# Kernel tuning notes

Hardware: AMD Instinct MI355X
Metric: run time of the kernel (lower is better)

## Reference

```python
import jax, jax.numpy as jnp
import numpy as np

B, T, C = 4, 2048, 1024
H, D = 16, 64  # num_heads, head_dim; H*D == C

def setup_inputs() -> dict:
    key = jax.random.key(0)
    ks = jax.random.split(key, 5)
    s = 0.02
    return {
        "x": jax.random.normal(ks[0], (B, T, C), dtype=jnp.float32),
        "W_qkv": jax.random.normal(ks[1], (C, 3 * C), dtype=jnp.float32) * s,
        "b_qkv": jnp.zeros((3 * C,), dtype=jnp.float32),
        "W_out": jax.random.normal(ks[2], (C, C), dtype=jnp.float32) * s,
        "b_out": jnp.zeros((C,), dtype=jnp.float32),
    }

def reference(x, W_qkv, b_qkv, W_out, b_out):
    Bx, Tx, Cx = x.shape
    qkv = x @ W_qkv + b_qkv                       # [B,T,3C]
    q, k, v = jnp.split(qkv, 3, axis=-1)
    def heads(t):
        return t.reshape(Bx, Tx, H, D).transpose(0, 2, 1, 3)  # [B,H,T,D]
    q, k, v = heads(q), heads(k), heads(v)
    scale = 1.0 / jnp.sqrt(jnp.float32(D))
    attn = jnp.einsum('bhqd,bhkd->bhqk', q, k) * scale
    causal = jnp.tril(jnp.ones((Tx, Tx), dtype=bool))  # True = keep
    attn = jnp.where(causal, attn, -jnp.inf)
    attn = jax.nn.softmax(attn, axis=-1)
    out = jnp.einsum('bhqk,bhkd->bhqd', attn, v)  # [B,H,T,D]
    out = out.transpose(0, 2, 1, 3).reshape(Bx, Tx, Cx)
    return out @ W_out + b_out
```

## Files before the change

### kernel.cpp

```cpp
#include <hip/hip_runtime.h>
#include <math.h>

typedef unsigned short u16;
using bf16x8   = __attribute__((ext_vector_type(8))) __bf16;
using floatx4  = __attribute__((ext_vector_type(4))) float;
using ushortx8 = __attribute__((ext_vector_type(8))) unsigned short;
using ushortx4 = __attribute__((ext_vector_type(4))) unsigned short;
using uintx4   = __attribute__((ext_vector_type(4))) unsigned int;

static __device__ __forceinline__ u16 f2bf(float f) {
  return (u16)((__float_as_uint(f) + 0x8000u) >> 16);
}
static __device__ __forceinline__ unsigned int pk2bf(float lo, float hi) {
  return __builtin_amdgcn_perm(__float_as_uint(hi) + 0x8000u,
                               __float_as_uint(lo) + 0x8000u, 0x07060302u);
}
static __device__ __forceinline__ void gload_lds16(const void* g, void* l) {
  __builtin_amdgcn_global_load_lds(
      (const __attribute__((address_space(1))) unsigned int*)g,
      (__attribute__((address_space(3))) unsigned int*)l, 16, 0, 0);
}

__global__ __launch_bounds__(256) void cvt_bf16(const float* __restrict__ x,
                                                u16* __restrict__ y) {
  const int i = (blockIdx.x * 256 + threadIdx.x) * 8;
  floatx4 f0 = *(const floatx4*)(x + i);
  floatx4 f1 = *(const floatx4*)(x + i + 4);
  uintx4 u;
  u[0] = pk2bf(f0[0], f0[1]); u[1] = pk2bf(f0[2], f0[3]);
  u[2] = pk2bf(f1[0], f1[1]); u[3] = pk2bf(f1[2], f1[3]);
  *(uintx4*)(y + i) = u;
}

__global__ __launch_bounds__(256) void transW(const float* __restrict__ W,
                                              u16* __restrict__ WT, int K, int N) {
  __shared__ float tile[64][68];
  const int t = threadIdx.x;
  const int kb = blockIdx.y * 64, nb = blockIdx.x * 64;
  {
    const int kl = t >> 2, nc = (t & 3) * 16;
    const float* src = W + (size_t)(kb + kl) * N + nb + nc;
    #pragma unroll
    for (int c = 0; c < 4; c++)
      *(floatx4*)&tile[kl][nc + c * 4] = *(const floatx4*)(src + c * 4);
  }
  __syncthreads();
  {
    const int nl = t >> 2, kc = (t & 3) * 16;
    uintx4 u0, u1;
    #pragma unroll
    for (int j = 0; j < 4; j++)
      u0[j] = pk2bf(tile[kc + 2 * j][nl], tile[kc + 2 * j + 1][nl]);
    #pragma unroll
    for (int j = 0; j < 4; j++)
      u1[j] = pk2bf(tile[kc + 8 + 2 * j][nl], tile[kc + 9 + 2 * j][nl]);
    u16* dst = WT + (size_t)(nb + nl) * K + kb + kc;
    *(uintx4*)dst = u0;
    *(uintx4*)(dst + 8) = u1;
  }
}

template <int OUT>
__global__ __launch_bounds__(256) void gemm128(
    const u16* __restrict__ A, const u16* __restrict__ Bt,
    const float* __restrict__ bias,
    u16* __restrict__ Qb, u16* __restrict__ Kb, u16* __restrict__ Vt,
    float* __restrict__ Out, int N, int K)
{
  __shared__ u16 As[128 * 64];
  __shared__ u16 Bs[128 * 64];

  const int tid  = threadIdx.x;
  const int wave = tid >> 6, lane = tid & 63;
  const int quad = lane >> 4, l15 = lane & 15;
  const int lrow = lane >> 3;
  const int scol = ((lane & 7) ^ lrow) * 8;

  const int rowBase = blockIdx.y * 128;
  const int colBase = blockIdx.x * 128;
  const int wRow = (wave >> 1) * 64;
  const int wCol = (wave & 1) * 64;

  floatx4 acc[4][4];
  #pragma unroll
  for (int mt = 0; mt < 4; mt++)
    #pragma unroll
    for (int nt = 0; nt < 4; nt++)
      acc[mt][nt] = floatx4{0.f, 0.f, 0.f, 0.f};

  const u16* Ap = A  + (size_t)(rowBase + (wave * 4) * 8 + lrow) * K + scol;
  const u16* Bp = Bt + (size_t)(colBase + (wave * 4) * 8 + lrow) * K + scol;

  for (int k0 = 0; k0 < K; k0 += 64) {
    __syncthreads();
    #pragma unroll
    for (int i = 0; i < 4; i++) {
      const int c = wave * 4 + i;
      gload_lds16(Ap + (size_t)(i * 8) * K + k0, &As[c * 512]);
      gload_lds16(Bp + (size_t)(i * 8) * K + k0, &Bs[c * 512]);
    }
    __syncthreads();

    #pragma unroll
    for (int ks = 0; ks < 2; ks++) {
      bf16x8 a[4], b[4];
      #pragma unroll
      for (int mt = 0; mt < 4; mt++) {
        const int row = wRow + mt * 16 + l15;
        a[mt] = *(const bf16x8*)&As[row * 64 + ((((ks << 2) | quad) ^ (l15 & 7)) << 3)];
      }
      #pragma unroll
      for (int nt = 0; nt < 4; nt++) {
        const int row = wCol + nt * 16 + l15;
        b[nt] = *(const bf16x8*)&Bs[row * 64 + ((((ks << 2) | quad) ^ (l15 & 7)) << 3)];
      }
      #pragma unroll
      for (int mt = 0; mt < 4; mt++)
        #pragma unroll
        for (int nt = 0; nt < 4; nt++)
          acc[mt][nt] = __builtin_amdgcn_mfma_f32_16x16x32_bf16(a[mt], b[nt], acc[mt][nt], 0, 0, 0);
    }
  }

  if constexpr (OUT == 0) {
    const int which = colBase >> 10;
    const int cb = colBase & 1023;
    const float qscale = 0.18033688011112042f;
    #pragma unroll
    for (int mt = 0; mt < 4; mt++) {
      const int gm0 = rowBase + wRow + mt * 16 + quad * 4;
      const int bb = gm0 >> 11, t0 = gm0 & 2047;
      #pragma unroll
      for (int nt = 0; nt < 4; nt++) {
        const int gn = colBase + wCol + nt * 16 + l15;
        const int gl = cb + wCol + nt * 16 + l15;
        const float bv = bias[gn];
        const int h = gl >> 6, d = gl & 63;
        const int bh = bb * 16 + h;
        if (which == 2) {
          ushortx4 pk;
          #pragma unroll
          for (int r = 0; r < 4; r++) pk[r] = f2bf(acc[mt][nt][r] + bv);
          *(ushortx4*)&Vt[((size_t)bh * 64 + d) * 2048 + t0] = pk;
        } else if (which == 0) {
          #pragma unroll
          for (int r = 0; r < 4; r++)
            Qb[((size_t)bh * 2048 + t0 + r) * 64 + d] = f2bf((acc[mt][nt][r] + bv) * qscale);
        } else {
          #pragma unroll
          for (int r = 0; r < 4; r++)
            Kb[((size_t)bh * 2048 + t0 + r) * 64 + d] = f2bf(acc[mt][nt][r] + bv);
        }
      }
    }
  } else {
    #pragma unroll
    for (int mt = 0; mt < 4; mt++)
      #pragma unroll
      for (int nt = 0; nt < 4; nt++) {
        const int gm = rowBase + wRow + mt * 16 + quad * 4;
        const int gn = colBase + wCol + nt * 16 + l15;
        const float bv = bias[gn];
        #pragma unroll
        for (int r = 0; r < 4; r++)
          Out[(size_t)(gm + r) * N + gn] = acc[mt][nt][r] + bv;
      }
  }
}

__global__ __launch_bounds__(256) void attn_fa(
    const u16* __restrict__ Qb, const u16* __restrict__ Kb,
    const u16* __restrict__ Vt, u16* __restrict__ Ob)
{
  __shared__ u16 Qs[128 * 64], Ks[64 * 64], Vs[64 * 64];
  __shared__ u16 Ps[4][32][72];

  const int tid  = threadIdx.x;
  const int wave = tid >> 6, lane = tid & 63;
  const int quad = lane >> 4, l15 = lane & 15;
  const int lrow = lane >> 3;
  const int scol = ((lane & 7) ^ lrow) * 8;

  const int bh    = blockIdx.x;
  const int qt    = 15 - (int)blockIdx.y;
  const int qbase = qt * 128;

  const u16* Qp = Qb + (size_t)bh * 2048 * 64;
  const u16* Kp = Kb + (size_t)bh * 2048 * 64;
  const u16* Vp = Vt + (size_t)bh * 64 * 2048;

  #pragma unroll
  for (int i = 0; i < 4; i++) {
    const int c = wave * 4 + i;
    gload_lds16(Qp + (size_t)(qbase + c * 8 + lrow) * 64 + scol, &Qs[c * 512]);
  }
  __syncthreads();

  const int swA0 = (quad ^ (l15 & 7)) * 8;
  const int swA1 = ((4 + quad) ^ (l15 & 7)) * 8;
  bf16x8 aq[2][2];
  #pragma unroll
  for (int mt = 0; mt < 2; mt++) {
    const int row = wave * 32 + mt * 16 + l15;
    aq[mt][0] = *(const bf16x8*)&Qs[row * 64 + swA0];
    aq[mt][1] = *(const bf16x8*)&Qs[row * 64 + swA1];
  }

  floatx4 o[2][4];
  #pragma unroll
  for (int mt = 0; mt < 2; mt++)
    #pragma unroll
    for (int dt = 0; dt < 4; dt++) o[mt][dt] = floatx4{0.f, 0.f, 0.f, 0.f};
  float lstat[2][4] = {{0.f, 0.f, 0.f, 0.f}, {0.f, 0.f, 0.f, 0.f}};

  const int rowmax = qbase + wave * 32 + 31;
  const int nk = 2 * qt + 2;
  for (int kt = 0; kt < nk; kt++) {
    const int kbase = kt * 64;
    __syncthreads();
    #pragma unroll
    for (int i = 0; i < 2; i++) {
      const int c = wave * 2 + i;
      gload_lds16(Kp + (size_t)(kbase + c * 8 + lrow) * 64 + scol, &Ks[c * 512]);
      gload_lds16(Vp + (size_t)(c * 8 + lrow) * 2048 + kbase + scol, &Vs[c * 512]);
    }
    __syncthreads();

    if (kbase > rowmax) continue;

    #pragma unroll
    for (int mt = 0; mt < 2; mt++) {
      const int rowmin = qbase + wave * 32 + mt * 16;
      const bool needmask = (kbase + 63 > rowmin);

      floatx4 s[4];
      #pragma unroll
      for (int ct = 0; ct < 4; ct++) {
        const int row = ct * 16 + l15;
        const bf16x8 b0 = *(const bf16x8*)&Ks[row * 64 + swA0];
        const bf16x8 b1 = *(const bf16x8*)&Ks[row * 64 + swA1];
        floatx4 z = floatx4{0.f, 0.f, 0.f, 0.f};
        z     = __builtin_amdgcn_mfma_f32_16x16x32_bf16(aq[mt][0], b0, z, 0, 0, 0);
        s[ct] = __builtin_amdgcn_mfma_f32_16x16x32_bf16(aq[mt][1], b1, z, 0, 0, 0);
      }

      #pragma unroll
      for (int r = 0; r < 4; r++) {
        const int qi = rowmin + quad * 4 + r;
        float ps = 0.f;
        #pragma unroll
        for (int ct = 0; ct < 4; ct++) {
          float p = exp2f(s[ct][r]);
          if (needmask && (kbase + ct * 16 + l15 > qi)) p = 0.f;
          ps += p;
          Ps[wave][mt * 16 + quad * 4 + r][ct * 16 + l15] = f2bf(p);
        }
        lstat[mt][r] += ps;
      }

      const bf16x8 pa0 = *(const bf16x8*)&Ps[wave][mt * 16 + l15][quad * 8];
      const bf16x8 pa1 = *(const bf16x8*)&Ps[wave][mt * 16 + l15][32 + quad * 8];
      #pragma unroll
      for (int dt = 0; dt < 4; dt++) {
        const int row = dt * 16 + l15;
        const bf16x8 v0 = *(const bf16x8*)&Vs[row * 64 + swA0];
        const bf16x8 v1 = *(const bf16x8*)&Vs[row * 64 + swA1];
        o[mt][dt] = __builtin_amdgcn_mfma_f32_16x16x32_bf16(pa0, v0, o[mt][dt], 0, 0, 0);
        o[mt][dt] = __builtin_amdgcn_mfma_f32_16x16x32_bf16(pa1, v1, o[mt][dt], 0, 0, 0);
      }
    }
  }

  const int bb = bh >> 4, h = bh & 15;
  #pragma unroll
  for (int mt = 0; mt < 2; mt++)
    #pragma unroll
    for (int r = 0; r < 4; r++) {
      float l = lstat[mt][r];
      #pragma unroll
      for (int off = 1; off < 16; off <<= 1) l += __shfl_xor(l, off, 16);
      const float linv = 1.0f / l;
      const int t = qbase + wave * 32 + mt * 16 + quad * 4 + r;
      #pragma unroll
      for (int dt = 0; dt < 4; dt++)
        Ob[((size_t)(bb * 2048 + t)) * 1024 + h * 64 + dt * 16 + l15] =
            f2bf(o[mt][dt][r] * linv);
    }
}

extern "C" void kernel_launch(void* const* d_in, const int* in_sizes, int n_in,
                              void* d_out, int out_size, void* d_ws, size_t ws_size,
                              hipStream_t stream) {
  const float* x    = (const float*)d_in[0];
  const float* Wqkv = (const float*)d_in[1];
  const float* bqkv = (const float*)d_in[2];
  const float* Wout = (const float*)d_in[3];
  const float* bout = (const float*)d_in[4];

  const size_t NB = (size_t)8192 * 1024;
  u16* Xb  = (u16*)d_ws;
  u16* WqT = Xb + NB;
  u16* Qb  = WqT + (size_t)3072 * 1024;
  u16* Kb  = Qb + NB;
  u16* Vt  = Kb + NB;

  cvt_bf16<<<4096, 256, 0, stream>>>(x, Xb);
  transW<<<dim3(48, 16), 256, 0, stream>>>(Wqkv, WqT, 1024, 3072);
  gemm128<0><<<dim3(24, 64), 256, 0, stream>>>(
      Xb, WqT, bqkv, Qb, Kb, Vt, nullptr, 3072, 1024);
  attn_fa<<<dim3(64, 16), 256, 0, stream>>>(Qb, Kb, Vt, Xb);
  transW<<<dim3(16, 16), 256, 0, stream>>>(Wout, WqT, 1024, 1024);
  gemm128<1><<<dim3(8, 64), 256, 0, stream>>>(
      Xb, WqT, bout, nullptr, nullptr, nullptr, (float*)d_out, 1024, 1024);
}
```

Baseline: 269.1 us.

## Compute transposed attention scores so P stores and output writes are vectorized

Swaps the MFMA operand order so each lane holds four consecutive key columns of S^T for one query row. P can then be written to LDS as packed 8-byte stores, row sums reduce with two shuffles instead of four, and the output is written as packed bf16 pairs. The separate P buffer is dropped and P now reuses the Q tile's LDS region after Q is moved into registers, which cuts LDS use and may help occupancy. A per-16-row causal skip is also added to avoid fully masked sub-tiles.

Measured after the change: 251.2 us. -6.6%, faster.

```diff
diff --git a/kernel.cpp b/kernel.cpp
--- a/kernel.cpp
+++ b/kernel.cpp
@@ -7,6 +7,7 @@
 using ushortx8 = __attribute__((ext_vector_type(8))) unsigned short;
 using ushortx4 = __attribute__((ext_vector_type(4))) unsigned short;
 using uintx4   = __attribute__((ext_vector_type(4))) unsigned int;
+using uintx2   = __attribute__((ext_vector_type(2))) unsigned int;
 
 static __device__ __forceinline__ u16 f2bf(float f) {
   return (u16)((__float_as_uint(f) + 0x8000u) >> 16);
@@ -172,8 +173,8 @@
     const u16* __restrict__ Qb, const u16* __restrict__ Kb,
     const u16* __restrict__ Vt, u16* __restrict__ Ob)
 {
-  __shared__ u16 Qs[128 * 64], Ks[64 * 64], Vs[64 * 64];
-  __shared__ u16 Ps[4][32][72];
+  __shared__ u16 Qs[128 * 64];
+  __shared__ u16 Ks[64 * 64], Vs[64 * 64];
 
   const int tid  = threadIdx.x;
   const int wave = tid >> 6, lane = tid & 63;
@@ -181,6 +182,8 @@
   const int lrow = lane >> 3;
   const int scol = ((lane & 7) ^ lrow) * 8;
 
+  u16* Pt = &Qs[wave * 16 * 72];
+
   const int bh    = blockIdx.x;
   const int qt    = 15 - (int)blockIdx.y;
   const int qbase = qt * 128;
@@ -211,7 +214,7 @@
   for (int mt = 0; mt < 2; mt++)
     #pragma unroll
     for (int dt = 0; dt < 4; dt++) o[mt][dt] = floatx4{0.f, 0.f, 0.f, 0.f};
-  float lstat[2][4] = {{0.f, 0.f, 0.f, 0.f}, {0.f, 0.f, 0.f, 0.f}};
+  float lsum[2] = {0.f, 0.f};
 
   const int rowmax = qbase + wave * 32 + 31;
   const int nk = 2 * qt + 2;
@@ -231,61 +234,71 @@
     #pragma unroll
     for (int mt = 0; mt < 2; mt++) {
       const int rowmin = qbase + wave * 32 + mt * 16;
+      if (kbase > rowmin + 15) continue;
       const bool needmask = (kbase + 63 > rowmin);
 
-      floatx4 s[4];
+      floatx4 st[4];
       #pragma unroll
       for (int ct = 0; ct < 4; ct++) {
         const int row = ct * 16 + l15;
-        const bf16x8 b0 = *(const bf16x8*)&Ks[row * 64 + swA0];
-        const bf16x8 b1 = *(const bf16x8*)&Ks[row * 64 + swA1];
+        const bf16x8 k0 = *(const bf16x8*)&Ks[row * 64 + swA0];
+        const bf16x8 k1 = *(const bf16x8*)&Ks[row * 64 + swA1];
         floatx4 z = floatx4{0.f, 0.f, 0.f, 0.f};
-        z     = __builtin_amdgcn_mfma_f32_16x16x32_bf16(aq[mt][0], b0, z, 0, 0, 0);
-        s[ct] = __builtin_amdgcn_mfma_f32_16x16x32_bf16(aq[mt][1], b1, z, 0, 0, 0);
-      }
-
-      #pragma unroll
-      for (int r = 0; r < 4; r++) {
-        const int qi = rowmin + quad * 4 + r;
-        float ps = 0.f;
-        #pragma unroll
-        for (int ct = 0; ct < 4; ct++) {
-          float p = exp2f(s[ct][r]);
-          if (needmask && (kbase + ct * 16 + l15 > qi)) p = 0.f;
-          ps += p;
-          Ps[wave][mt * 16 + quad * 4 + r][ct * 16 + l15] = f2bf(p);
+        z      = __builtin_amdgcn_mfma_f32_16x16x32_bf16(k0, aq[mt][0], z, 0, 0, 0);
+        st[ct] = __builtin_amdgcn_mfma_f32_16x16x32_bf16(k1, aq[mt][1], z, 0, 0, 0);
+      }
+
+      const int qg = rowmin + l15;
+      float ls = 0.f;
+      #pragma unroll
+      for (int ct = 0; ct < 4; ct++) {
+        float p0 = exp2f(st[ct][0]), p1 = exp2f(st[ct][1]);
+        float p2 = exp2f(st[ct][2]), p3 = exp2f(st[ct][3]);
+        if (needmask) {
+          const int k0i = kbase + ct * 16 + quad * 4;
+          if (k0i + 0 > qg) p0 = 0.f;
+          if (k0i + 1 > qg) p1 = 0.f;
+          if (k0i + 2 > qg) p2 = 0.f;
+          if (k0i + 3 > qg) p3 = 0.f;
         }
-        lstat[mt][r] += ps;
-      }
-
-      const bf16x8 pa0 = *(const bf16x8*)&Ps[wave][mt * 16 + l15][quad * 8];
-      const bf16x8 pa1 = *(const bf16x8*)&Ps[wave][mt * 16 + l15][32 + quad * 8];
+        ls += (p0 + p1) + (p2 + p3);
+        uintx2 w;
+        w[0] = pk2bf(p0, p1);
+        w[1] = pk2bf(p2, p3);
+        *(uintx2*)&Pt[l15 * 72 + ct * 16 + quad * 4] = w;
+      }
+      lsum[mt] += ls;
+
+      const bf16x8 pb0 = *(const bf16x8*)&Pt[l15 * 72 + quad * 8];
+      const bf16x8 pb1 = *(const bf16x8*)&Pt[l15 * 72 + 32 + quad * 8];
       #pragma unroll
       for (int dt = 0; dt < 4; dt++) {
         const int row = dt * 16 + l15;
         const bf16x8 v0 = *(const bf16x8*)&Vs[row * 64 + swA0];
         const bf16x8 v1 = *(const bf16x8*)&Vs[row * 64 + swA1];
-        o[mt][dt] = __builtin_amdgcn_mfma_f32_16x16x32_bf16(pa0, v0, o[mt][dt], 0, 0, 0);
-        o[mt][dt] = __builtin_amdgcn_mfma_f32_16x16x32_bf16(pa1, v1, o[mt][dt], 0, 0, 0);
+        o[mt][dt] = __builtin_amdgcn_mfma_f32_16x16x32_bf16(v0, pb0, o[mt][dt], 0, 0, 0);
+        o[mt][dt] = __builtin_amdgcn_mfma_f32_16x16x32_bf16(v1, pb1, o[mt][dt], 0, 0, 0);
       }
     }
   }
 
   const int bb = bh >> 4, h = bh & 15;
   #pragma unroll
-  for (int mt = 0; mt < 2; mt++)
-    #pragma unroll
-    for (int r = 0; r < 4; r++) {
-      float l = lstat[mt][r];
-      #pragma unroll
-      for (int off = 1; off < 16; off <<= 1) l += __shfl_xor(l, off, 16);
-      const float linv = 1.0f / l;
-      const int t = qbase + wave * 32 + mt * 16 + quad * 4 + r;
-      #pragma unroll
-      for (int dt = 0; dt < 4; dt++)
-        Ob[((size_t)(bb * 2048 + t)) * 1024 + h * 64 + dt * 16 + l15] =
-            f2bf(o[mt][dt][r] * linv);
-    }
+  for (int mt = 0; mt < 2; mt++) {
+    float l = lsum[mt];
+    l += __shfl_xor(l, 16);
+    l += __shfl_xor(l, 32);
+    const float linv = 1.0f / l;
+    const int t = qbase + wave * 32 + mt * 16 + l15;
+    u16* dst = Ob + ((size_t)(bb * 2048 + t)) * 1024 + h * 64 + quad * 4;
+    #pragma unroll
+    for (int dt = 0; dt < 4; dt++) {
+      uintx2 w;
+      w[0] = pk2bf(o[mt][dt][0] * linv, o[mt][dt][1] * linv);
+      w[1] = pk2bf(o[mt][dt][2] * linv, o[mt][dt][3] * linv);
+      *(uintx2*)(dst + dt * 16) = w;
+    }
+  }
 }
 
 extern "C" void kernel_launch(void* const* d_in, const int* in_sizes, int n_in,
```
